# Optimization experiments

Measured on AMD Instinct MI355X. Metric: run time of the kernel, lower is better.

## Reference

```python
import jax, jax.numpy as jnp
import numpy as np

N_NODES = 50000
C = 128
E = 800000
B = 4096
NEG = 5
NUM_LAYERS = 3


def setup_inputs() -> dict:
    key = jax.random.key(0)
    ks = jax.random.split(key, 8)
    edge_index = jax.random.randint(ks[0], (2, E), 0, N_NODES, dtype=jnp.int64)
    edge_weight = jax.random.uniform(ks[1], (E,), dtype=jnp.float32)
    n_id = jax.random.randint(ks[2], ((2 + NEG) * B,), 0, N_NODES, dtype=jnp.int64)
    x = jnp.zeros((1,), jnp.float32)  # ignored by forward (overwritten by id_embed)
    id_embed = jax.random.normal(ks[3], (N_NODES, C), jnp.float32) * 0.1
    w1 = jax.random.normal(ks[4], (2 * C, C), jnp.float32) * (1.0 / np.sqrt(2 * C))
    b1 = jnp.zeros((C,), jnp.float32)
    w2 = jax.random.normal(ks[5], (C, 1), jnp.float32) * (1.0 / np.sqrt(C))
    b2 = jnp.zeros((1,), jnp.float32)
    return {"x": x, "edge_index": edge_index, "edge_weight": edge_weight,
            "n_id": n_id, "neg_sample_num": NEG, "id_embed": id_embed,
            "w1": w1, "b1": b1, "w2": w2, "b2": b2}


def reference(x, edge_index, edge_weight, n_id, neg_sample_num, id_embed, w1, b1, w2, b2):
    n_nodes = id_embed.shape[0]
    row, col = edge_index[0], edge_index[1]
    # symmetric GCN normalization (LGCConv)
    deg = jax.ops.segment_sum(jnp.ones_like(row, dtype=id_embed.dtype), row,
                              num_segments=n_nodes)
    dinv = jnp.where(deg > 0, jax.lax.rsqrt(jnp.maximum(deg, 1e-12)), 0.0)
    norm = (dinv[row] * dinv[col])[:, None]  # [E,1]
    h = id_embed
    final = id_embed
    for _ in range(NUM_LAYERS):
        h = jax.ops.segment_sum(norm * h[col], row, num_segments=n_nodes)
        final = final + h
    final = final / (NUM_LAYERS + 1)
    # split n_id into (out, pos, neg) index groups
    b = n_id.shape[0] // (2 + neg_sample_num)
    out = final[n_id[:b]]
    pos = final[n_id[b:2 * b]]
    neg = final[n_id[2 * b:]]
    tiled_out = jnp.repeat(out, neg_sample_num, axis=0)  # [b*neg, C]

    def pred_head(z):  # Linear -> LeakyReLU(0.2) -> (Dropout eval=identity) -> Linear
        z = jax.nn.leaky_relu(z @ w1 + b1, negative_slope=0.2)
        return z @ w2 + b2

    pos_logit = pred_head(jnp.concatenate([out, pos], axis=-1))
    neg_logits = pred_head(jnp.concatenate([tiled_out, neg], axis=-1))
    return pos_logit, neg_logits
```

## Files before the change

kernel.cpp:

```cpp
#include <hip/hip_runtime.h>
#include <hip/hip_bf16.h>

#define C 128
#define NBKT 128
#define BCAP 8192

typedef __bf16 bf16x8 __attribute__((ext_vector_type(8)));
typedef float floatx4 __attribute__((ext_vector_type(4)));

__device__ __forceinline__ unsigned short f2bf(float f) {
    unsigned u = __float_as_uint(f);
    unsigned r = (u + 0x7FFFu + ((u >> 16) & 1u)) >> 16;
    return (unsigned short)r;
}
__device__ __forceinline__ float bflo(unsigned v) { return __uint_as_float(v << 16); }
__device__ __forceinline__ float bfhi(unsigned v) { return __uint_as_float(v & 0xFFFF0000u); }
__device__ __forceinline__ unsigned packbf(float lo, float hi) {
    return (unsigned)f2bf(lo) | ((unsigned)f2bf(hi) << 16);
}

__device__ __forceinline__ int g_idx(const void* p, long long i, int is64) {
    if (is64) return (int)((const long long*)p)[i];
    return ((const int*)p)[i];
}
__device__ __forceinline__ float g_flt(const void* p, long long i, int isf32) {
    if (isf32) return ((const float*)p)[i];
    return __uint_as_float(((unsigned)((const unsigned short*)p)[i]) << 16);
}

__global__ void k_bucketA(const void* edge, int E, int rpb,
                          unsigned* __restrict__ bucketbuf, int* __restrict__ bucketcnt) {
    __shared__ int lcnt[NBKT];
    __shared__ int lbase[NBKT];
    __shared__ int sflag;
    int t = threadIdx.x;
    if (t < 64) {
        const unsigned* wrd = (const unsigned*)edge;
        int predA = (t < 32) ? (wrd[2 * t + 1] == 0u) : 1;
        unsigned long long mA = __ballot(predA);
        if (t == 0) sflag = (mA == ~0ull) ? 1 : 0;
    }
    __syncthreads();
    int is64 = sflag;
    const int PER = 8;
    int chunkSz = blockDim.x * PER;
    long long stride = (long long)gridDim.x * chunkSz;
    for (long long base = (long long)blockIdx.x * chunkSz; base < E; base += stride) {
        if (t < NBKT) lcnt[t] = 0;
        __syncthreads();
        int bkt[PER], rank[PER];
        unsigned enc[PER];
        long long e0 = base + (long long)t * PER;
        int rr[PER], cc[PER];
        if (e0 + PER <= E) {
            if (is64) {
                const long long* pr = (const long long*)edge + e0;
                const long long* pc = (const long long*)edge + E + e0;
#pragma unroll
                for (int j = 0; j < PER; j += 2) {
                    longlong2 vr = *(const longlong2*)(pr + j);
                    longlong2 vc = *(const longlong2*)(pc + j);
                    rr[j] = (int)vr.x; rr[j + 1] = (int)vr.y;
                    cc[j] = (int)vc.x; cc[j + 1] = (int)vc.y;
                }
            } else {
                const int* pr = (const int*)edge + e0;
                const int* pc = (const int*)edge + E + e0;
#pragma unroll
                for (int j = 0; j < PER; j += 4) {
                    int4 vr = *(const int4*)(pr + j);
                    int4 vc = *(const int4*)(pc + j);
                    rr[j] = vr.x; rr[j + 1] = vr.y; rr[j + 2] = vr.z; rr[j + 3] = vr.w;
                    cc[j] = vc.x; cc[j + 1] = vc.y; cc[j + 2] = vc.z; cc[j + 3] = vc.w;
                }
            }
#pragma unroll
            for (int j = 0; j < PER; ++j) {
                int b = rr[j] / rpb;
                bkt[j] = b;
                enc[j] = ((unsigned)(rr[j] - b * rpb) << 16) | (unsigned)(cc[j] & 0xFFFF);
                rank[j] = atomicAdd(&lcnt[b], 1);
            }
        } else {
#pragma unroll
            for (int j = 0; j < PER; ++j) {
                long long e = e0 + j;
                if (e < E) {
                    int r = g_idx(edge, e, is64);
                    int c = g_idx(edge, (long long)E + e, is64);
                    int b = r / rpb;
                    bkt[j] = b;
                    enc[j] = ((unsigned)(r - b * rpb) << 16) | (unsigned)(c & 0xFFFF);
                    rank[j] = atomicAdd(&lcnt[b], 1);
                } else bkt[j] = -1;
            }
        }
        __syncthreads();
        if (t < NBKT) lbase[t] = atomicAdd(&bucketcnt[t], lcnt[t]);
        __syncthreads();
#pragma unroll
        for (int j = 0; j < PER; ++j) {
            if (bkt[j] >= 0) {
                int pos = lbase[bkt[j]] + rank[j];
                if (pos < BCAP)
                    bucketbuf[(size_t)bkt[j] * BCAP + pos] = enc[j];
            }
        }
    }
}

__global__ __launch_bounds__(512) void k_bsort(
        const unsigned* __restrict__ bucketbuf, const int* __restrict__ bucketcnt,
        int* __restrict__ rowptr, float* __restrict__ dinv, float* __restrict__ di2,
        float* __restrict__ rdinv, unsigned short* __restrict__ cols16, int N, int rpb) {
    __shared__ int hist[512];
    int b = blockIdx.x;
    int t = threadIdx.x;
    int base = 0, cnt = 0, total = 0;
    for (int i = 0; i < NBKT; ++i) {
        int v = bucketcnt[i];
        if (v > BCAP) v = BCAP;
        if (i < b) base += v;
        if (i == b) cnt = v;
        total += v;
    }
    int r0 = b * rpb;
    int rows = N - r0;
    if (rows > rpb) rows = rpb;
    if (rows < 0) rows = 0;

    hist[t] = 0;
    __syncthreads();
    const unsigned* buf = bucketbuf + (size_t)b * BCAP;
    for (int i = t; i < cnt; i += 512) atomicAdd(&hist[buf[i] >> 16], 1);
    __syncthreads();
    int v = hist[t];
    __syncthreads();
    for (int off = 1; off < 512; off <<= 1) {
        int x = (t >= off) ? hist[t - off] : 0;
        __syncthreads();
        hist[t] += x;
        __syncthreads();
    }
    int excl = hist[t] - v;
    if (t < rows) {
        int r = r0 + t;
        rowptr[r] = base + excl;
        float fd = (float)v;
        float dv = (v > 0) ? rsqrtf(fd) : 0.0f;
        dinv[r] = dv;
        di2[r] = dv * dv;
        rdinv[r] = (v > 0) ? sqrtf(fd) : 0.0f;
    }
    if (b == NBKT - 1 && t == 0) rowptr[N] = total;
    __syncthreads();
    hist[t] = base + excl;
    __syncthreads();
    for (int i = t; i < cnt; i += 512) {
        unsigned u = buf[i];
        int pos = atomicAdd(&hist[u >> 16], 1);
        cols16[pos] = (unsigned short)(u & 0xFFFF);
    }
}

__global__ void k_initprep(const void* emb, const float* __restrict__ dinv,
                           unsigned* __restrict__ h0, unsigned* __restrict__ g0,
                           unsigned* __restrict__ g1, unsigned* __restrict__ g2,
                           int n2, int SST,
                           const void* w1, const void* b1, const void* w2, const void* b2,
                           unsigned short* __restrict__ w1t, float* __restrict__ b1f,
                           float* __restrict__ w2f, float* __restrict__ b2f,
                           const void* n_id, int nids, unsigned char* __restrict__ mark) {
    __shared__ int sf32, sid;
    int t = threadIdx.x;
    if (t < 64) {
        const unsigned short* h = (const unsigned short*)emb;
        int ex = (h[2 * t] >> 7) & 0xFF;
        unsigned long long mP = __ballot(ex >= 0x6C && ex <= 0x7F);
        const unsigned* nw = (const unsigned*)n_id;
        int predB = (t < 32) ? (nw[2 * t + 1] == 0u) : 1;
        unsigned long long mB = __ballot(predB);
        if (t == 0) {
            sf32 = (__popcll(mP) < 32) ? 1 : 0;
            sid = (mB == ~0ull) ? 1 : 0;
        }
    }
    __syncthreads();
    int f32 = sf32, id64 = sid;
    int i = blockIdx.x * blockDim.x + t;
    if (i < n2) {
        float lo = g_flt(emb, 2LL * i, f32);
        float hi = g_flt(emb, 2LL * i + 1, f32);
        int n = i >> 6, w = i & 63;
        size_t o = (size_t)(w >> 5) * SST + (size_t)n * 32 + (w & 31);
        h0[o] = packbf(lo, hi);
        float dv = dinv[n];
        g0[o] = packbf(lo * dv, hi * dv);
    }
    if (i < nids) mark[g_idx(n_id, i, id64)] = 1;
    if (i < 256 * 128) {
        int k = i >> 7, n = i & 127;
        w1t[n * 256 + k] = f2bf(g_flt(w1, i, f32));
    }
    if (i < 128) {
        b1f[i] = g_flt(b1, i, f32);
        w2f[i] = g_flt(w2, i, f32);
    }
    if (i == 0) b2f[0] = g_flt(b2, 0, f32);
    if (i < 64) {
        int s = i >> 5, w = i & 31;
        size_t o = (size_t)s * SST + (size_t)(n2 >> 6) * 32 + w;
        g0[o] = 0u; g1[o] = 0u; g2[o] = 0u;
    }
}

__global__ __launch_bounds__(256) void k_compact(const unsigned char* __restrict__ mark, int N,
                                                 int* __restrict__ cnt, int* __restrict__ clist) {
    __shared__ int wbase[4];
    int n = blockIdx.x * blockDim.x + threadIdx.x;
    int m = (n < N) ? (mark[n] ? 1 : 0) : 0;
    int lane = threadIdx.x & 63, wave = threadIdx.x >> 6;
    unsigned long long bal = __ballot(m);
    int rank = __popcll(bal & ((1ull << lane) - 1ull));
    if (lane == 0) wbase[wave] = __popcll(bal);
    __syncthreads();
    if (threadIdx.x == 0) {
        int tot = wbase[0] + wbase[1] + wbase[2] + wbase[3];
        int b0 = atomicAdd(cnt, tot);
        int acc = b0;
#pragma unroll
        for (int w = 0; w < 4; ++w) { int c = wbase[w]; wbase[w] = acc; acc += c; }
    }
    __syncthreads();
    if (m) clist[wbase[wave] + rank] = n;
}

__global__ void k_layer(const int* __restrict__ rowptr, const unsigned short* __restrict__ cols16,
                        const uint4* __restrict__ gin, uint4* __restrict__ gout,
                        const float* __restrict__ di2, int N, int SSTU4) {
    int b = blockIdx.x;
    int slice = (b >> 2) & 1;
    int tile = ((b >> 3) << 2) | (b & 3);
    int node = tile * 32 + (threadIdx.x >> 3);
    if (node >= N) return;
    int l8 = threadIdx.x & 7;
    const uint4* gs = gin + (size_t)slice * SSTU4;
    int p = rowptr[node];
    int end = rowptr[node + 1];
    float a0 = 0.f, a1 = 0.f, a2 = 0.f, a3 = 0.f;
    float a4 = 0.f, a5 = 0.f, a6 = 0.f, a7 = 0.f;
    for (int base = p; base < end; base += 8) {
        int c[8];
#pragma unroll
        for (int j = 0; j < 8; ++j) {
            int idx = base + j;
            int cv = cols16[idx];
            c[j] = (idx < end) ? cv : N;
        }
#pragma unroll
        for (int j = 0; j < 8; ++j) {
            uint4 v = gs[(size_t)c[j] * 8 + l8];
            a0 += bflo(v.x); a1 += bfhi(v.x);
            a2 += bflo(v.y); a3 += bfhi(v.y);
            a4 += bflo(v.z); a5 += bfhi(v.z);
            a6 += bflo(v.w); a7 += bfhi(v.w);
        }
    }
    float s = di2[node];
    uint4 o;
    o.x = packbf(a0 * s, a1 * s);
    o.y = packbf(a2 * s, a3 * s);
    o.z = packbf(a4 * s, a5 * s);
    o.w = packbf(a6 * s, a7 * s);
    gout[(size_t)slice * SSTU4 + (size_t)node * 8 + l8] = o;
}

__global__ void k_layer3(const int* __restrict__ rowptr, const unsigned short* __restrict__ cols16,
                         const uint4* __restrict__ gin , const uint4* __restrict__ h0,
                         const uint4* __restrict__ g1, uint4* __restrict__ fin,
                         const float* __restrict__ di2, const float* __restrict__ rdinv,
                         const int* __restrict__ cnt, const int* __restrict__ clist,
                         int N, int SSTU4, int TILES_PER) {
    int b = blockIdx.x;
    int slice = (b >> 2) & 1;
    int tile = ((b >> 3) << 2) | (b & 3);
    int nsub = threadIdx.x >> 3;
    int l8 = threadIdx.x & 7;
    int cntv = *cnt;
    size_t sb = (size_t)slice * SSTU4;
    const uint4* gs = gin + sb;
    for (int tl = tile; tl * 32 < cntv; tl += TILES_PER) {
        int li = tl * 32 + nsub;
        if (li < cntv) {
            int node = clist[li];
            int p = rowptr[node], end = rowptr[node + 1];
            float a0 = 0.f, a1 = 0.f, a2 = 0.f, a3 = 0.f;
            float a4 = 0.f, a5 = 0.f, a6 = 0.f, a7 = 0.f;
            for (int base = p; base < end; base += 8) {
                int c[8];
#pragma unroll
                for (int j = 0; j < 8; ++j) {
                    int idx = base + j;
                    int cv = cols16[idx];
                    c[j] = (idx < end) ? cv : N;
                }
#pragma unroll
                for (int j = 0; j < 8; ++j) {
                    uint4 v = gs[(size_t)c[j] * 8 + l8];
                    a0 += bflo(v.x); a1 += bfhi(v.x);
                    a2 += bflo(v.y); a3 += bfhi(v.y);
                    a4 += bflo(v.z); a5 += bfhi(v.z);
                    a6 += bflo(v.w); a7 += bfhi(v.w);
                }
            }
            float s = di2[node];
            float rd = rdinv[node];
            size_t ro = (size_t)node * 8 + l8;
            uint4 x0 = h0[sb + ro];
            uint4 x1 = g1[sb + ro];
            uint4 x2 = gs[ro];
            uint4 o;
            o.x = packbf(0.25f * (bflo(x0.x) + rd * (bflo(x1.x) + bflo(x2.x) + s * a0)),
                         0.25f * (bfhi(x0.x) + rd * (bfhi(x1.x) + bfhi(x2.x) + s * a1)));
            o.y = packbf(0.25f * (bflo(x0.y) + rd * (bflo(x1.y) + bflo(x2.y) + s * a2)),
                         0.25f * (bfhi(x0.y) + rd * (bfhi(x1.y) + bfhi(x2.y) + s * a3)));
            o.z = packbf(0.25f * (bflo(x0.z) + rd * (bflo(x1.z) + bflo(x2.z) + s * a4)),
                         0.25f * (bfhi(x0.z) + rd * (bfhi(x1.z) + bfhi(x2.z) + s * a5)));
            o.w = packbf(0.25f * (bflo(x0.w) + rd * (bflo(x1.w) + bflo(x2.w) + s * a6)),
                         0.25f * (bfhi(x0.w) + rd * (bfhi(x1.w) + bfhi(x2.w) + s * a7)));
            fin[(size_t)node * 16 + slice * 8 + l8] = o;
        }
    }
}

__global__ void k_head(const uint4* __restrict__ fin, const void* n_id,
                       const unsigned short* __restrict__ w1t,
                       const float* __restrict__ b1f, const float* __restrict__ w2f,
                       const float* __restrict__ b2f,
                       float* __restrict__ out, int B, int NEG) {
    __shared__ unsigned short z[64][264];
    __shared__ int sid;
    int t = threadIdx.x;
    if (t < 64) {
        const unsigned* nw = (const unsigned*)n_id;
        int predB = (t < 32) ? (nw[2 * t + 1] == 0u) : 1;
        unsigned long long mB = __ballot(predB);
        if (t == 0) sid = (mB == ~0ull) ? 1 : 0;
    }
    __syncthreads();
    int id64 = sid;
    int mbase = blockIdx.x * 64;

#pragma unroll
    for (int i = 0; i < 8; ++i) {
        int flat = i * 256 + t;
        int m = flat >> 5;
        int q = flat & 31;
        int gm = mbase + m;
        int r;
        if (gm < B) {
            r = (q < 16) ? g_idx(n_id, gm, id64) : g_idx(n_id, B + gm, id64);
        } else {
            int j = gm - B;
            r = (q < 16) ? g_idx(n_id, j / NEG, id64) : g_idx(n_id, 2 * B + j, id64);
        }
        uint4 v = fin[(size_t)r * 16 + (q & 15)];
        *(uint4*)((char*)&z[m][0] + q * 16) = v;
    }
    __syncthreads();

    int wave = t >> 6, lane = t & 63;
    int quad = lane >> 4, l16 = lane & 15;

    floatx4 acc[8] = {};
    bf16x8 a[8];
    const unsigned short* zrow = &z[wave * 16 + l16][0];
#pragma unroll
    for (int ks = 0; ks < 8; ++ks)
        a[ks] = *(const bf16x8*)(zrow + ks * 32 + quad * 8);

#pragma unroll
    for (int ks = 0; ks < 8; ++ks) {
#pragma unroll
        for (int nt = 0; nt < 8; ++nt) {
            bf16x8 b = *(const bf16x8*)(w1t + (nt * 16 + l16) * 256 + ks * 32 + quad * 8);
            acc[nt] = __builtin_amdgcn_mfma_f32_16x16x32_bf16(a[ks], b, acc[nt], 0, 0, 0);
        }
    }

    float s0 = 0.f, s1 = 0.f, s2 = 0.f, s3 = 0.f;
#pragma unroll
    for (int nt = 0; nt < 8; ++nt) {
        int col = nt * 16 + l16;
        float bb = b1f[col], ww = w2f[col];
        float v0 = acc[nt][0] + bb; v0 = (v0 > 0.f) ? v0 : 0.2f * v0; s0 += v0 * ww;
        float v1 = acc[nt][1] + bb; v1 = (v1 > 0.f) ? v1 : 0.2f * v1; s1 += v1 * ww;
        float v2 = acc[nt][2] + bb; v2 = (v2 > 0.f) ? v2 : 0.2f * v2; s2 += v2 * ww;
        float v3 = acc[nt][3] + bb; v3 = (v3 > 0.f) ? v3 : 0.2f * v3; s3 += v3 * ww;
    }
#pragma unroll
    for (int off = 1; off <= 8; off <<= 1) {
        s0 += __shfl_xor(s0, off, 64);
        s1 += __shfl_xor(s1, off, 64);
        s2 += __shfl_xor(s2, off, 64);
        s3 += __shfl_xor(s3, off, 64);
    }
    if (l16 == 0) {
        int rowbase = mbase + wave * 16 + quad * 4;
        float bb2 = b2f[0];
        out[rowbase + 0] = s0 + bb2;
        out[rowbase + 1] = s1 + bb2;
        out[rowbase + 2] = s2 + bb2;
        out[rowbase + 3] = s3 + bb2;
    }
}

extern "C" void kernel_launch(void* const* d_in, const int* in_sizes, int n_in,
                              void* d_out, int out_size, void* d_ws, size_t ws_size,
                              hipStream_t stream) {
    const void* edge_index = d_in[1];
    const void* n_id       = d_in[3];
    const void* id_embed   = d_in[5];
    const void* w1 = d_in[6];
    const void* b1 = d_in[7];
    const void* w2 = d_in[8];
    const void* b2 = d_in[9];
    float* out = (float*)d_out;

    const int E  = in_sizes[1] / 2;
    const int N  = in_sizes[5] / C;
    const int NEG = 5;
    const int B  = in_sizes[3] / (2 + NEG);
    const int nids = (2 + NEG) * B;
    const int n_out_rows = B + B * NEG;
    const int SST = (N + 1) * 32;
    const int SSTU4 = (N + 1) * 8;
    const int NB = 2 * SST;
    const int rpb = (N + NBKT - 1) / NBKT;

    size_t off = 0;
    auto alloc = [&](size_t nf) {
        char* p = (char*)d_ws + off * 4;
        off += (nf + 255) & ~(size_t)255;
        return p;
    };
    int*   bucketcnt = (int*)alloc(NBKT);
    unsigned char* mark = (unsigned char*)alloc((N + 3) / 4);
    int*   clist     = (int*)alloc(N);
    float* dinv      = (float*)alloc(N + 1);
    float* di2       = (float*)alloc(N);
    float* rdinv     = (float*)alloc(N);
    int*   rowptr    = (int*)alloc(N + 1);
    unsigned short* cols16 = (unsigned short*)alloc(((size_t)E + 16 + 1) / 2);
    unsigned* bucketbuf = (unsigned*)alloc((size_t)NBKT * BCAP);
    unsigned* h0     = (unsigned*)alloc(NB);
    unsigned* g0     = (unsigned*)alloc(NB);
    unsigned* g1     = (unsigned*)alloc(NB);
    unsigned* g2     = (unsigned*)alloc(NB);
    unsigned* fin    = (unsigned*)alloc((size_t)N * 64);
    unsigned short* w1t = (unsigned short*)alloc(256 * 128 / 2);
    float* b1f       = (float*)alloc(C);
    float* w2f       = (float*)alloc(C);
    float* b2f       = (float*)alloc(8);
    int*   ccnt      = bucketcnt + 128;

    const int BS = 256;
    hipMemsetAsync(bucketcnt, 0, 1024 + (size_t)N, stream);

    const int gridA = (E + BS * 8 - 1) / (BS * 8);
    k_bucketA<<<gridA, BS, 0, stream>>>(edge_index, E, rpb, bucketbuf, bucketcnt);
    k_bsort<<<NBKT, 512, 0, stream>>>(bucketbuf, bucketcnt, rowptr, dinv, di2, rdinv,
                                      cols16, N, rpb);
    k_initprep<<<(N * 64 + BS - 1) / BS, BS, 0, stream>>>(
        id_embed, dinv, h0, g0, g1, g2, N * 64, SST, w1, b1, w2, b2,
        w1t, b1f, w2f, b2f, n_id, nids, mark);
    k_compact<<<(N + BS - 1) / BS, BS, 0, stream>>>(mark, N, ccnt, clist);

    const int tiles = (N + 31) / 32;
    const int layer_grid = 8 * ((tiles + 3) / 4);
    const int TILES_PER = 4 * ((tiles + 3) / 4);
    k_layer<<<layer_grid, BS, 0, stream>>>(rowptr, cols16, (const uint4*)g0, (uint4*)g1,
                                           di2, N, SSTU4);
    k_layer<<<layer_grid, BS, 0, stream>>>(rowptr, cols16, (const uint4*)g1, (uint4*)g2,
                                           di2, N, SSTU4);
    k_layer3<<<layer_grid, BS, 0, stream>>>(rowptr, cols16, (const uint4*)g2, (const uint4*)h0,
                                            (const uint4*)g1, (uint4*)fin, di2, rdinv,
                                            ccnt, clist, N, SSTU4, TILES_PER);

    k_head<<<n_out_rows / 64, BS, 0, stream>>>((const uint4*)fin, n_id, w1t, b1f, w2f, b2f,
                                               out, B, NEG);
}
```

Measured before the change: 212.2 us.

## Process graph nodes in degree-sorted order to balance SpMM layer work

Builds a degree histogram inside the bucket sort, scans it, and counting-sorts the nodes by degree into an order array. The layer kernels and the compaction of marked nodes then walk nodes in that order, so the 8-lane groups in a wave handle rows of similar length and divergence on the per-row edge loops drops. This adds two small kernels plus global atomics. Consecutive groups now hit scattered rows, so the rowptr and output writes lose locality.

```diff
diff --git a/kernel.cpp b/kernel.cpp
--- a/kernel.cpp
+++ b/kernel.cpp
@@ -112,7 +112,8 @@
 __global__ __launch_bounds__(512) void k_bsort(
         const unsigned* __restrict__ bucketbuf, const int* __restrict__ bucketcnt,
         int* __restrict__ rowptr, float* __restrict__ dinv, float* __restrict__ di2,
-        float* __restrict__ rdinv, unsigned short* __restrict__ cols16, int N, int rpb) {
+        float* __restrict__ rdinv, unsigned short* __restrict__ cols16,
+        int* __restrict__ deg, int* __restrict__ dh, int N, int rpb) {
     __shared__ int hist[512];
     int b = blockIdx.x;
     int t = threadIdx.x;
@@ -146,6 +147,8 @@
     if (t < rows) {
         int r = r0 + t;
         rowptr[r] = base + excl;
+        deg[r] = v;
+        atomicAdd(&dh[v > 1023 ? 1023 : v], 1);
         float fd = (float)v;
         float dv = (v > 0) ? rsqrtf(fd) : 0.0f;
         dinv[r] = dv;
@@ -160,6 +163,32 @@
         unsigned u = buf[i];
         int pos = atomicAdd(&hist[u >> 16], 1);
         cols16[pos] = (unsigned short)(u & 0xFFFF);
+    }
+}
+
+__global__ __launch_bounds__(1024) void k_dscan(const int* __restrict__ dh,
+                                                int* __restrict__ dcur) {
+    __shared__ int s[1024];
+    int t = threadIdx.x;
+    int v = dh[t];
+    s[t] = v;
+    __syncthreads();
+    for (int off = 1; off < 1024; off <<= 1) {
+        int x = (t >= off) ? s[t - off] : 0;
+        __syncthreads();
+        s[t] += x;
+        __syncthreads();
+    }
+    dcur[t] = s[t] - v;
+}
+
+__global__ void k_place(const int* __restrict__ deg, int N,
+                        int* __restrict__ dcur, int* __restrict__ order) {
+    int n = blockIdx.x * blockDim.x + threadIdx.x;
+    if (n < N) {
+        int d = deg[n]; if (d > 1023) d = 1023;
+        int pos = atomicAdd(&dcur[d], 1);
+        order[pos] = n;
     }
 }
 
@@ -214,11 +243,13 @@
     }
 }
 
-__global__ __launch_bounds__(256) void k_compact(const unsigned char* __restrict__ mark, int N,
+__global__ __launch_bounds__(256) void k_compact(const unsigned char* __restrict__ mark,
+                                                 const int* __restrict__ order, int N,
                                                  int* __restrict__ cnt, int* __restrict__ clist) {
     __shared__ int wbase[4];
-    int n = blockIdx.x * blockDim.x + threadIdx.x;
-    int m = (n < N) ? (mark[n] ? 1 : 0) : 0;
+    int i = blockIdx.x * blockDim.x + threadIdx.x;
+    int n = (i < N) ? order[i] : -1;
+    int m = (n >= 0) ? (mark[n] ? 1 : 0) : 0;
     int lane = threadIdx.x & 63, wave = threadIdx.x >> 6;
     unsigned long long bal = __ballot(m);
     int rank = __popcll(bal & ((1ull << lane) - 1ull));
@@ -236,13 +267,15 @@
 }
 
 __global__ void k_layer(const int* __restrict__ rowptr, const unsigned short* __restrict__ cols16,
+                        const int* __restrict__ order,
                         const uint4* __restrict__ gin, uint4* __restrict__ gout,
                         const float* __restrict__ di2, int N, int SSTU4) {
     int b = blockIdx.x;
     int slice = (b >> 2) & 1;
     int tile = ((b >> 3) << 2) | (b & 3);
-    int node = tile * 32 + (threadIdx.x >> 3);
-    if (node >= N) return;
+    int pos = tile * 32 + (threadIdx.x >> 3);
+    if (pos >= N) return;
+    int node = order[pos];
     int l8 = threadIdx.x & 7;
     const uint4* gs = gin + (size_t)slice * SSTU4;
     int p = rowptr[node];
@@ -446,6 +479,10 @@
     };
     int*   bucketcnt = (int*)alloc(NBKT);
     unsigned char* mark = (unsigned char*)alloc((N + 3) / 4);
+    int*   dh        = (int*)alloc(1024);
+    int*   dcur      = (int*)alloc(1024);
+    int*   deg       = (int*)alloc(N);
+    int*   order     = (int*)alloc(N);
     int*   clist     = (int*)alloc(N);
     float* dinv      = (float*)alloc(N + 1);
     float* di2       = (float*)alloc(N);
@@ -465,24 +502,27 @@
     int*   ccnt      = bucketcnt + 128;
 
     const int BS = 256;
-    hipMemsetAsync(bucketcnt, 0, 1024 + (size_t)N, stream);
+    size_t zlen = (size_t)((char*)deg - (char*)bucketcnt);
+    hipMemsetAsync(bucketcnt, 0, zlen, stream);
 
     const int gridA = (E + BS * 8 - 1) / (BS * 8);
     k_bucketA<<<gridA, BS, 0, stream>>>(edge_index, E, rpb, bucketbuf, bucketcnt);
     k_bsort<<<NBKT, 512, 0, stream>>>(bucketbuf, bucketcnt, rowptr, dinv, di2, rdinv,
-                                      cols16, N, rpb);
+                                      cols16, deg, dh, N, rpb);
+    k_dscan<<<1, 1024, 0, stream>>>(dh, dcur);
+    k_place<<<(N + BS - 1) / BS, BS, 0, stream>>>(deg, N, dcur, order);
     k_initprep<<<(N * 64 + BS - 1) / BS, BS, 0, stream>>>(
         id_embed, dinv, h0, g0, g1, g2, N * 64, SST, w1, b1, w2, b2,
         w1t, b1f, w2f, b2f, n_id, nids, mark);
-    k_compact<<<(N + BS - 1) / BS, BS, 0, stream>>>(mark, N, ccnt, clist);
+    k_compact<<<(N + BS - 1) / BS, BS, 0, stream>>>(mark, order, N, ccnt, clist);
 
     const int tiles = (N + 31) / 32;
     const int layer_grid = 8 * ((tiles + 3) / 4);
     const int TILES_PER = 4 * ((tiles + 3) / 4);
-    k_layer<<<layer_grid, BS, 0, stream>>>(rowptr, cols16, (const uint4*)g0, (uint4*)g1,
-                                           di2, N, SSTU4);
-    k_layer<<<layer_grid, BS, 0, stream>>>(rowptr, cols16, (const uint4*)g1, (uint4*)g2,
-                                           di2, N, SSTU4);
+    k_layer<<<layer_grid, BS, 0, stream>>>(rowptr, cols16, order, (const uint4*)g0,
+                                           (uint4*)g1, di2, N, SSTU4);
+    k_layer<<<layer_grid, BS, 0, stream>>>(rowptr, cols16, order, (const uint4*)g1,
+                                           (uint4*)g2, di2, N, SSTU4);
     k_layer3<<<layer_grid, BS, 0, stream>>>(rowptr, cols16, (const uint4*)g2, (const uint4*)h0,
                                             (const uint4*)g1, (uint4*)fin, di2, rdinv,
                                             ccnt, clist, N, SSTU4, TILES_PER);
```

Result: slower. 480.8 us (+126.5%).

## Double sort buckets and precompute bucket offsets in a prefix kernel

Applied to the files above, without the earlier changes.

Raises the bucket count from 128 to 256, so the per-bucket sort kernel runs twice as many smaller blocks and fills more of the GPU's compute units. A small single-block kernel now computes the exclusive prefix of bucket counts once. This replaces the serial loop over all bucket counts that every sort thread used to run. The cost is one extra kernel launch and a reworked workspace layout and memset range.

```diff
diff --git a/kernel.cpp b/kernel.cpp
--- a/kernel.cpp
+++ b/kernel.cpp
@@ -2,7 +2,7 @@
 #include <hip/hip_bf16.h>
 
 #define C 128
-#define NBKT 128
+#define NBKT 256
 #define BCAP 8192
 
 typedef __bf16 bf16x8 __attribute__((ext_vector_type(8)));
@@ -109,21 +109,35 @@
     }
 }
 
+__global__ __launch_bounds__(NBKT) void k_pfx(const int* __restrict__ bucketcnt,
+                                              int* __restrict__ bktbase) {
+    __shared__ int s[NBKT];
+    int t = threadIdx.x;
+    int v = bucketcnt[t];
+    if (v > BCAP) v = BCAP;
+    s[t] = v;
+    __syncthreads();
+    for (int off = 1; off < NBKT; off <<= 1) {
+        int x = (t >= off) ? s[t - off] : 0;
+        __syncthreads();
+        s[t] += x;
+        __syncthreads();
+    }
+    bktbase[t] = s[t] - v;
+    if (t == NBKT - 1) bktbase[NBKT] = s[t];
+}
+
 __global__ __launch_bounds__(512) void k_bsort(
         const unsigned* __restrict__ bucketbuf, const int* __restrict__ bucketcnt,
+        const int* __restrict__ bktbase,
         int* __restrict__ rowptr, float* __restrict__ dinv, float* __restrict__ di2,
         float* __restrict__ rdinv, unsigned short* __restrict__ cols16, int N, int rpb) {
     __shared__ int hist[512];
     int b = blockIdx.x;
     int t = threadIdx.x;
-    int base = 0, cnt = 0, total = 0;
-    for (int i = 0; i < NBKT; ++i) {
-        int v = bucketcnt[i];
-        if (v > BCAP) v = BCAP;
-        if (i < b) base += v;
-        if (i == b) cnt = v;
-        total += v;
-    }
+    int base = bktbase[b];
+    int cnt = bucketcnt[b];
+    if (cnt > BCAP) cnt = BCAP;
     int r0 = b * rpb;
     int rows = N - r0;
     if (rows > rpb) rows = rpb;
@@ -152,7 +166,7 @@
         di2[r] = dv * dv;
         rdinv[r] = (v > 0) ? sqrtf(fd) : 0.0f;
     }
-    if (b == NBKT - 1 && t == 0) rowptr[N] = total;
+    if (b == NBKT - 1 && t == 0) rowptr[N] = bktbase[NBKT];
     __syncthreads();
     hist[t] = base + excl;
     __syncthreads();
@@ -445,7 +459,9 @@
         return p;
     };
     int*   bucketcnt = (int*)alloc(NBKT);
+    int*   ccnt      = (int*)alloc(8);
     unsigned char* mark = (unsigned char*)alloc((N + 3) / 4);
+    int*   bktbase   = (int*)alloc(NBKT + 1);
     int*   clist     = (int*)alloc(N);
     float* dinv      = (float*)alloc(N + 1);
     float* di2       = (float*)alloc(N);
@@ -462,15 +478,16 @@
     float* b1f       = (float*)alloc(C);
     float* w2f       = (float*)alloc(C);
     float* b2f       = (float*)alloc(8);
-    int*   ccnt      = bucketcnt + 128;
 
     const int BS = 256;
-    hipMemsetAsync(bucketcnt, 0, 1024 + (size_t)N, stream);
+    size_t zlen = (size_t)((char*)bktbase - (char*)bucketcnt);
+    hipMemsetAsync(bucketcnt, 0, zlen, stream);
 
     const int gridA = (E + BS * 8 - 1) / (BS * 8);
     k_bucketA<<<gridA, BS, 0, stream>>>(edge_index, E, rpb, bucketbuf, bucketcnt);
-    k_bsort<<<NBKT, 512, 0, stream>>>(bucketbuf, bucketcnt, rowptr, dinv, di2, rdinv,
-                                      cols16, N, rpb);
+    k_pfx<<<1, NBKT, 0, stream>>>(bucketcnt, bktbase);
+    k_bsort<<<NBKT, 512, 0, stream>>>(bucketbuf, bucketcnt, bktbase, rowptr, dinv, di2,
+                                      rdinv, cols16, N, rpb);
     k_initprep<<<(N * 64 + BS - 1) / BS, BS, 0, stream>>>(
         id_embed, dinv, h0, g0, g1, g2, N * 64, SST, w1, b1, w2, b2,
         w1t, b1f, w2f, b2f, n_id, nids, mark);
```

Measured after the change: 209.3 us, median of 2. Within noise of the previous version (-1.4%).
